# Performance work log

Measured on AMD Instinct MI355X. Metric: run time of the kernel, lower is better.

## Reference

```python
import jax, jax.numpy as jnp
import numpy as np

E, K, H, I = 64, 8, 2048, 768  # num_experts, top_k, hidden, moe_intermediate

def setup_inputs() -> dict:
    key = jax.random.key(0)
    k1, k2, k3, k4 = jax.random.split(key, 4)
    return {
        "hidden_states": jax.random.normal(k1, (1, 1024, H), dtype=jnp.float32),
        "w_gate": jax.random.normal(k2, (H, E), dtype=jnp.float32) * 0.02,
        "w13": jax.random.normal(k3, (E, H, 2 * I), dtype=jnp.float32) * 0.02,  # fused gate+up proj
        "w2": jax.random.normal(k4, (E, I, H), dtype=jnp.float32) * 0.02,
    }

def reference(hidden_states, w_gate, w13, w2):
    orig_shape = hidden_states.shape
    x = hidden_states.reshape(-1, orig_shape[-1])            # [T, H]
    T = x.shape[0]

    # Router: logits -> softmax -> top-k -> renormalize (norm_topk_prob=True)
    router_logits = x @ w_gate                               # [T, E]
    probs = jax.nn.softmax(router_logits, axis=-1)
    topk_w, topk_idx = jax.lax.top_k(probs, K)               # [T, K]
    topk_w = topk_w / jnp.sum(topk_w, axis=-1, keepdims=True)
    # Dense combine-weight matrix [T, E] (zero for non-routed experts)
    combine = jnp.zeros((T, E), dtype=x.dtype).at[
        jnp.arange(T)[:, None], topk_idx].add(topk_w)

    # Expert SwiGLU FFN, computed densely for all experts, masked by combine
    h = jnp.einsum('th,ehd->etd', x, w13)                    # [E, T, 2I]
    gate, up = h[..., :I], h[..., I:]
    act = jax.nn.silu(gate) * up                             # [E, T, I]
    y = jnp.einsum('eti,eih->eth', act, w2)                  # [E, T, H]
    out = jnp.einsum('eth,te->th', y, combine)               # [T, H]
    return out.reshape(orig_shape)
```

## Files before the change

### kernel.cpp

```cpp
#include <hip/hip_runtime.h>
#include <hip/hip_bf16.h>
#include <math.h>

#define NE 64
#define NK 8
#define NH 2048
#define NI 768
#define NT 1024
#define APITCH 40

typedef float f32x4 __attribute__((ext_vector_type(4)));
typedef __bf16 bf16x8 __attribute__((ext_vector_type(8)));
typedef __bf16 bf16x4 __attribute__((ext_vector_type(4)));

__global__ __launch_bounds__(256) void router_k(
    const float* __restrict__ x, const float* __restrict__ wg,
    __bf16* __restrict__ x_bf, int* __restrict__ topk_idx,
    float* __restrict__ topk_w)
{
    __shared__ float xs[4][NH];
    const int wave = threadIdx.x >> 6;
    const int lane = threadIdx.x & 63;
    const int t = blockIdx.x * 4 + wave;

    const float* xrow = x + (size_t)t * NH;
    __bf16* brow = x_bf + (size_t)t * NH;
    #pragma unroll
    for (int j = 0; j < 8; ++j) {
        int idx = j * 256 + lane * 4;
        f32x4 v = *reinterpret_cast<const f32x4*>(xrow + idx);
        *reinterpret_cast<f32x4*>(&xs[wave][idx]) = v;
        bf16x4 b;
        b[0] = (__bf16)v.x; b[1] = (__bf16)v.y; b[2] = (__bf16)v.z; b[3] = (__bf16)v.w;
        *reinterpret_cast<bf16x4*>(brow + idx) = b;
    }
    __syncthreads();

    float a0 = 0.f, a1 = 0.f, a2 = 0.f, a3 = 0.f;
    for (int h = 0; h < NH; h += 4) {
        a0 = fmaf(xs[wave][h + 0], wg[(h + 0) * NE + lane], a0);
        a1 = fmaf(xs[wave][h + 1], wg[(h + 1) * NE + lane], a1);
        a2 = fmaf(xs[wave][h + 2], wg[(h + 2) * NE + lane], a2);
        a3 = fmaf(xs[wave][h + 3], wg[(h + 3) * NE + lane], a3);
    }
    float acc = (a0 + a1) + (a2 + a3);

    float cur = acc;
    float sel_v[NK]; int sel_i[NK];
    #pragma unroll
    for (int k = 0; k < NK; ++k) {
        float bv = cur; int bi = lane;
        #pragma unroll
        for (int s = 32; s; s >>= 1) {
            float ov = __shfl_xor(bv, s, 64);
            int   oi = __shfl_xor(bi, s, 64);
            if (ov > bv || (ov == bv && oi < bi)) { bv = ov; bi = oi; }
        }
        sel_v[k] = bv; sel_i[k] = bi;
        if (lane == bi) cur = -3.4e38f;
    }
    float m = sel_v[0];
    float ssum = 0.f;
    #pragma unroll
    for (int k = 0; k < NK; ++k) ssum += expf(sel_v[k] - m);

    if (lane < NK) {
        float w = expf(sel_v[lane] - m) / ssum;
        topk_idx[t * NK + lane] = sel_i[lane];
        topk_w[t * NK + lane] = w;
    }
}

__global__ __launch_bounds__(256) void scanscatter_k(
    const int* __restrict__ topk_idx, const float* __restrict__ topk_w,
    int* __restrict__ counts, int* __restrict__ offs,
    int* __restrict__ slot_tok, float* __restrict__ slot_w,
    int* __restrict__ slot_of)
{
    __shared__ int hist[NE], base[NE], cur[NE];
    const int tid = threadIdx.x;
    if (tid < NE) hist[tid] = 0;
    __syncthreads();
    for (int i = tid; i < NT * NK; i += 256)
        atomicAdd(&hist[topk_idx[i]], 1);
    __syncthreads();
    if (tid == 0) {
        int r = 0;
        for (int e = 0; e < NE; ++e) { base[e] = r; r += hist[e]; }
    }
    __syncthreads();
    if (tid < NE) { counts[tid] = hist[tid]; offs[tid] = base[tid]; cur[tid] = 0; }
    __syncthreads();
    for (int i = tid; i < NT * NK; i += 256) {
        int e = topk_idx[i];
        int p = atomicAdd(&cur[e], 1);
        int g = base[e] + p;
        slot_tok[g] = i >> 3;
        slot_w[g] = topk_w[i];
        slot_of[i] = g;
    }
}

__global__ __launch_bounds__(256, 2) void e1_k(
    const __bf16* __restrict__ x_bf, const float* __restrict__ w13,
    const int* __restrict__ counts, const int* __restrict__ offs,
    const int* __restrict__ slot_tok, __bf16* __restrict__ act)
{
    const int e = blockIdx.x;
    const int cnt = counts[e];
    const int m0 = blockIdx.z * 256;
    if (m0 >= cnt) return;
    const int rows = min(256, cnt - m0);
    const int n0 = blockIdx.y * 64;
    const int goff = offs[e] + m0;

    __shared__ __bf16 A[2][256 * APITCH];
    __shared__ __bf16 B[2][128 * APITCH];
    __shared__ int tok[256];

    const int tid = threadIdx.x;
    tok[tid] = (tid < rows) ? slot_tok[goff + tid] : 0;
    __syncthreads();

    const int wave = tid >> 6, lane = tid & 63;
    f32x4 acc[4][8];
    #pragma unroll
    for (int i = 0; i < 4; ++i)
        #pragma unroll
        for (int j = 0; j < 8; ++j) acc[i][j] = (f32x4){0.f, 0.f, 0.f, 0.f};

    const float* w13e = w13 + (size_t)e * NH * (2 * NI);
    const int cc = tid & 31, kch = tid >> 5;
    const int bcol0 = cc * 4;
    const int gcol = (bcol0 < 64) ? (n0 + bcol0) : (NI + n0 + bcol0 - 64);
    const int rot = (cc >> 1) & 3;

    const __bf16* aptr[4];
    int aoff[4];
    bool aok[4];
    #pragma unroll
    for (int it = 0; it < 4; ++it) {
        int item = it * 256 + tid;
        int r = item >> 2, ch = item & 3;
        aptr[it] = x_bf + (size_t)tok[r] * NH + ch * 8;
        aoff[it] = r * APITCH + ch * 8;
        aok[it] = (r < rows);
    }
    const float* bptr = w13e + (size_t)(kch * 4) * (2 * NI) + gcol;
    int bcol[4], boff[4];
    #pragma unroll
    for (int jj = 0; jj < 4; ++jj) {
        int j = (jj + rot) & 3;
        bcol[jj] = j;
        boff[jj] = (bcol0 + j) * APITCH + kch * 4;
    }

    bf16x8 aReg[4];
    f32x4 bReg[4];

    auto loadT = [&](int kk) {
        #pragma unroll
        for (int it = 0; it < 4; ++it)
            if (aok[it]) aReg[it] = *reinterpret_cast<const bf16x8*>(aptr[it] + kk);
        #pragma unroll
        for (int ki = 0; ki < 4; ++ki)
            bReg[ki] = *reinterpret_cast<const f32x4*>(bptr + (size_t)(kk + ki) * (2 * NI));
    };
    auto writeT = [&](int buf) {
        #pragma unroll
        for (int it = 0; it < 4; ++it)
            if (aok[it]) *reinterpret_cast<bf16x8*>(&A[buf][aoff[it]]) = aReg[it];
        #pragma unroll
        for (int jj = 0; jj < 4; ++jj) {
            int j = bcol[jj];
            bf16x4 p;
            p[0] = (__bf16)bReg[0][j]; p[1] = (__bf16)bReg[1][j];
            p[2] = (__bf16)bReg[2][j]; p[3] = (__bf16)bReg[3][j];
            *reinterpret_cast<bf16x4*>(&B[buf][boff[jj]]) = p;
        }
    };
    auto compute = [&](int buf) {
        bf16x8 bfr[8];
        #pragma unroll
        for (int nf = 0; nf < 8; ++nf) {
            int col = nf * 16 + (lane & 15);
            bfr[nf] = *reinterpret_cast<const bf16x8*>(
                &B[buf][col * APITCH + (lane >> 4) * 8]);
        }
        #pragma unroll
        for (int mf = 0; mf < 4; ++mf) {
            int rf = mf * 64 + wave * 16;
            if (rf < rows) {
                int row = rf + (lane & 15);
                bf16x8 a = *reinterpret_cast<const bf16x8*>(
                    &A[buf][row * APITCH + (lane >> 4) * 8]);
                #pragma unroll
                for (int nf = 0; nf < 8; ++nf)
                    acc[mf][nf] = __builtin_amdgcn_mfma_f32_16x16x32_bf16(
                        a, bfr[nf], acc[mf][nf], 0, 0, 0);
            }
        }
    };

    loadT(0);
    writeT(0);
    __syncthreads();

    #pragma unroll 1
    for (int t = 0; t < 64; ++t) {
        if (t + 1 < 64) loadT((t + 1) * 32);
        compute(t & 1);
        if (t + 1 < 64) writeT((t + 1) & 1);
        __syncthreads();
    }

    #pragma unroll
    for (int mf = 0; mf < 4; ++mf) {
        int rf = mf * 64 + wave * 16;
        if (rf >= rows) continue;
        #pragma unroll
        for (int nf = 0; nf < 4; ++nf) {
            f32x4 g = acc[mf][nf];
            f32x4 u = acc[mf][nf + 4];
            int col = n0 + nf * 16 + (lane & 15);
            #pragma unroll
            for (int r = 0; r < 4; ++r) {
                int row = rf + ((lane >> 4) << 2) + r;
                if (row < rows) {
                    float gv = g[r];
                    float a = gv / (1.f + expf(-gv)) * u[r];
                    act[(size_t)(goff + row) * NI + col] = (__bf16)a;
                }
            }
        }
    }
}

__global__ __launch_bounds__(256, 2) void e2_k(
    const __bf16* __restrict__ act, const float* __restrict__ w2,
    const int* __restrict__ counts, const int* __restrict__ offs,
    const float* __restrict__ slot_w, __bf16* __restrict__ partial)
{
    const int e = blockIdx.x;
    const int cnt = counts[e];
    const int m0 = blockIdx.z * 256;
    if (m0 >= cnt) return;
    const int rows = min(256, cnt - m0);
    const int n0 = blockIdx.y * 128;
    const int goff = offs[e] + m0;

    __shared__ __bf16 A[2][256 * APITCH];
    __shared__ __bf16 B[2][128 * APITCH];

    const int tid = threadIdx.x, wave = tid >> 6, lane = tid & 63;
    f32x4 acc[4][8];
    #pragma unroll
    for (int i = 0; i < 4; ++i)
        #pragma unroll
        for (int j = 0; j < 8; ++j) acc[i][j] = (f32x4){0.f, 0.f, 0.f, 0.f};

    const float* w2e = w2 + (size_t)e * NI * NH;
    const int cc = tid & 31, kch = tid >> 5;
    const int bcol0 = cc * 4;
    const int rot = (cc >> 1) & 3;

    const __bf16* aptr[4];
    int aoff[4];
    bool aok[4];
    #pragma unroll
    for (int it = 0; it < 4; ++it) {
        int item = it * 256 + tid;
        int r = item >> 2, ch = item & 3;
        aptr[it] = act + (size_t)(goff + r) * NI + ch * 8;
        aoff[it] = r * APITCH + ch * 8;
        aok[it] = (r < rows);
    }
    const float* bptr = w2e + (size_t)(kch * 4) * NH + n0 + bcol0;
    int bcol[4], boff[4];
    #pragma unroll
    for (int jj = 0; jj < 4; ++jj) {
        int j = (jj + rot) & 3;
        bcol[jj] = j;
        boff[jj] = (bcol0 + j) * APITCH + kch * 4;
    }

    bf16x8 aReg[4];
    f32x4 bReg[4];

    auto loadT = [&](int kk) {
        #pragma unroll
        for (int it = 0; it < 4; ++it)
            if (aok[it]) aReg[it] = *reinterpret_cast<const bf16x8*>(aptr[it] + kk);
        #pragma unroll
        for (int ki = 0; ki < 4; ++ki)
            bReg[ki] = *reinterpret_cast<const f32x4*>(bptr + (size_t)(kk + ki) * NH);
    };
    auto writeT = [&](int buf) {
        #pragma unroll
        for (int it = 0; it < 4; ++it)
            if (aok[it]) *reinterpret_cast<bf16x8*>(&A[buf][aoff[it]]) = aReg[it];
        #pragma unroll
        for (int jj = 0; jj < 4; ++jj) {
            int j = bcol[jj];
            bf16x4 p;
            p[0] = (__bf16)bReg[0][j]; p[1] = (__bf16)bReg[1][j];
            p[2] = (__bf16)bReg[2][j]; p[3] = (__bf16)bReg[3][j];
            *reinterpret_cast<bf16x4*>(&B[buf][boff[jj]]) = p;
        }
    };
    auto compute = [&](int buf) {
        bf16x8 bfr[8];
        #pragma unroll
        for (int nf = 0; nf < 8; ++nf) {
            int col = nf * 16 + (lane & 15);
            bfr[nf] = *reinterpret_cast<const bf16x8*>(
                &B[buf][col * APITCH + (lane >> 4) * 8]);
        }
        #pragma unroll
        for (int mf = 0; mf < 4; ++mf) {
            int rf = mf * 64 + wave * 16;
            if (rf < rows) {
                int row = rf + (lane & 15);
                bf16x8 a = *reinterpret_cast<const bf16x8*>(
                    &A[buf][row * APITCH + (lane >> 4) * 8]);
                #pragma unroll
                for (int nf = 0; nf < 8; ++nf)
                    acc[mf][nf] = __builtin_amdgcn_mfma_f32_16x16x32_bf16(
                        a, bfr[nf], acc[mf][nf], 0, 0, 0);
            }
        }
    };

    loadT(0);
    writeT(0);
    __syncthreads();

    #pragma unroll 1
    for (int t = 0; t < 24; ++t) {
        if (t + 1 < 24) loadT((t + 1) * 32);
        compute(t & 1);
        if (t + 1 < 24) writeT((t + 1) & 1);
        __syncthreads();
    }

    #pragma unroll
    for (int mf = 0; mf < 4; ++mf) {
        int rf = mf * 64 + wave * 16;
        if (rf >= rows) continue;
        int rb = rf + ((lane >> 4) << 2);
        #pragma unroll
        for (int r = 0; r < 4; ++r) {
            int row = rb + r;
            if (row >= rows) continue;
            int gs = goff + row;
            float wv = slot_w[gs];
            #pragma unroll
            for (int nf = 0; nf < 8; ++nf) {
                int col = n0 + nf * 16 + (lane & 15);
                partial[(size_t)gs * NH + col] = (__bf16)(wv * acc[mf][nf][r]);
            }
        }
    }
}

__global__ __launch_bounds__(256) void combine_k(
    const __bf16* __restrict__ partial, const int* __restrict__ slot_of,
    float* __restrict__ out)
{
    const int t = blockIdx.x;
    const int c0 = threadIdx.x * 8;
    __shared__ int gs[NK];
    if (threadIdx.x < NK) gs[threadIdx.x] = slot_of[t * NK + threadIdx.x];
    __syncthreads();

    float s[8] = {0.f, 0.f, 0.f, 0.f, 0.f, 0.f, 0.f, 0.f};
    #pragma unroll
    for (int k = 0; k < NK; ++k) {
        bf16x8 v = *reinterpret_cast<const bf16x8*>(partial + (size_t)gs[k] * NH + c0);
        #pragma unroll
        for (int j = 0; j < 8; ++j) s[j] += (float)v[j];
    }
    f32x4 o0 = {s[0], s[1], s[2], s[3]};
    f32x4 o1 = {s[4], s[5], s[6], s[7]};
    *reinterpret_cast<f32x4*>(out + (size_t)t * NH + c0) = o0;
    *reinterpret_cast<f32x4*>(out + (size_t)t * NH + c0 + 4) = o1;
}

extern "C" void kernel_launch(void* const* d_in, const int* in_sizes, int n_in,
                              void* d_out, int out_size, void* d_ws, size_t ws_size,
                              hipStream_t stream)
{
    const float* x   = (const float*)d_in[0];
    const float* wg  = (const float*)d_in[1];
    const float* w13 = (const float*)d_in[2];
    const float* w2  = (const float*)d_in[3];
    float* out = (float*)d_out;
    char* ws = (char*)d_ws;

    __bf16* x_bf = (__bf16*)ws;
    size_t o = (size_t)4 * 1024 * 1024;
    __bf16* act = (__bf16*)(ws + o);      o += (size_t)8192 * NI * 2;
    __bf16* partial = (__bf16*)(ws + o);  o += (size_t)8192 * NH * 2;
    int*   topk_idx = (int*)(ws + o);     o += 8192 * 4;
    float* topk_w   = (float*)(ws + o);   o += 8192 * 4;
    int*   slot_tok = (int*)(ws + o);     o += 8192 * 4;
    float* slot_w   = (float*)(ws + o);   o += 8192 * 4;
    int*   slot_of  = (int*)(ws + o);     o += 8192 * 4;
    int*   counts   = (int*)(ws + o);     o += 256;
    int*   offs     = (int*)(ws + o);     o += 256;

    router_k    <<<NT / 4, 256, 0, stream>>>(x, wg, x_bf, topk_idx, topk_w);
    scanscatter_k<<<1, 256, 0, stream>>>(topk_idx, topk_w, counts, offs,
                                         slot_tok, slot_w, slot_of);
    e1_k<<<dim3(NE, NI / 64, 2), 256, 0, stream>>>(x_bf, w13, counts, offs, slot_tok, act);
    e2_k<<<dim3(NE, NH / 128, 2), 256, 0, stream>>>(act, w2, counts, offs, slot_w, partial);
    combine_k<<<NT, 256, 0, stream>>>(partial, slot_of, out);
}
```

Before: 438.4 us.

## Load A fragments directly from global and double K-step per LDS stage

```diff
diff --git a/kernel.cpp b/kernel.cpp
--- a/kernel.cpp
+++ b/kernel.cpp
@@ -7,7 +7,8 @@
 #define NH 2048
 #define NI 768
 #define NT 1024
-#define APITCH 40
+#define BP 40
+#define BSUB (128 * BP)
 
 typedef float f32x4 __attribute__((ext_vector_type(4)));
 typedef __bf16 bf16x8 __attribute__((ext_vector_type(8)));
@@ -114,12 +115,11 @@
     const int n0 = blockIdx.y * 64;
     const int goff = offs[e] + m0;
 
-    __shared__ __bf16 A[2][256 * APITCH];
-    __shared__ __bf16 B[2][128 * APITCH];
+    __shared__ __bf16 B[2][2 * BSUB];
     __shared__ int tok[256];
 
     const int tid = threadIdx.x;
-    tok[tid] = (tid < rows) ? slot_tok[goff + tid] : 0;
+    tok[tid] = (tid < rows) ? slot_tok[goff + tid] : slot_tok[goff];
     __syncthreads();
 
     const int wave = tid >> 6, lane = tid & 63;
@@ -128,78 +128,76 @@
     for (int i = 0; i < 4; ++i)
         #pragma unroll
         for (int j = 0; j < 8; ++j) acc[i][j] = (f32x4){0.f, 0.f, 0.f, 0.f};
+
+    const __bf16* ap[4];
+    bool mok[4];
+    #pragma unroll
+    for (int mf = 0; mf < 4; ++mf) {
+        int rf = mf * 64 + wave * 16;
+        mok[mf] = (rf < rows);
+        int arow = rf + (lane & 15);
+        ap[mf] = x_bf + (size_t)tok[arow] * NH + ((lane >> 4) << 3);
+    }
 
     const float* w13e = w13 + (size_t)e * NH * (2 * NI);
     const int cc = tid & 31, kch = tid >> 5;
     const int bcol0 = cc * 4;
     const int gcol = (bcol0 < 64) ? (n0 + bcol0) : (NI + n0 + bcol0 - 64);
     const int rot = (cc >> 1) & 3;
-
-    const __bf16* aptr[4];
-    int aoff[4];
-    bool aok[4];
-    #pragma unroll
-    for (int it = 0; it < 4; ++it) {
-        int item = it * 256 + tid;
-        int r = item >> 2, ch = item & 3;
-        aptr[it] = x_bf + (size_t)tok[r] * NH + ch * 8;
-        aoff[it] = r * APITCH + ch * 8;
-        aok[it] = (r < rows);
-    }
     const float* bptr = w13e + (size_t)(kch * 4) * (2 * NI) + gcol;
-    int bcol[4], boff[4];
+    int bj[4], boff[4];
     #pragma unroll
     for (int jj = 0; jj < 4; ++jj) {
         int j = (jj + rot) & 3;
-        bcol[jj] = j;
-        boff[jj] = (bcol0 + j) * APITCH + kch * 4;
-    }
-
-    bf16x8 aReg[4];
-    f32x4 bReg[4];
-
+        bj[jj] = j;
+        boff[jj] = (bcol0 + j) * BP + kch * 4;
+    }
+
+    f32x4 bReg[2][4];
     auto loadT = [&](int kk) {
         #pragma unroll
-        for (int it = 0; it < 4; ++it)
-            if (aok[it]) aReg[it] = *reinterpret_cast<const bf16x8*>(aptr[it] + kk);
-        #pragma unroll
-        for (int ki = 0; ki < 4; ++ki)
-            bReg[ki] = *reinterpret_cast<const f32x4*>(bptr + (size_t)(kk + ki) * (2 * NI));
+        for (int s = 0; s < 2; ++s)
+            #pragma unroll
+            for (int ki = 0; ki < 4; ++ki)
+                bReg[s][ki] = *reinterpret_cast<const f32x4*>(
+                    bptr + (size_t)(kk + s * 32 + ki) * (2 * NI));
     };
     auto writeT = [&](int buf) {
         #pragma unroll
-        for (int it = 0; it < 4; ++it)
-            if (aok[it]) *reinterpret_cast<bf16x8*>(&A[buf][aoff[it]]) = aReg[it];
-        #pragma unroll
-        for (int jj = 0; jj < 4; ++jj) {
-            int j = bcol[jj];
-            bf16x4 p;
-            p[0] = (__bf16)bReg[0][j]; p[1] = (__bf16)bReg[1][j];
-            p[2] = (__bf16)bReg[2][j]; p[3] = (__bf16)bReg[3][j];
-            *reinterpret_cast<bf16x4*>(&B[buf][boff[jj]]) = p;
+        for (int s = 0; s < 2; ++s)
+            #pragma unroll
+            for (int jj = 0; jj < 4; ++jj) {
+                int j = bj[jj];
+                bf16x4 p;
+                p[0] = (__bf16)bReg[s][0][j]; p[1] = (__bf16)bReg[s][1][j];
+                p[2] = (__bf16)bReg[s][2][j]; p[3] = (__bf16)bReg[s][3][j];
+                *reinterpret_cast<bf16x4*>(&B[buf][s * BSUB + boff[jj]]) = p;
+            }
+    };
+    auto compute = [&](int buf) {
+        #pragma unroll
+        for (int kk = 0; kk < 2; ++kk) {
+            bf16x8 av[4];
+            #pragma unroll
+            for (int mf = 0; mf < 4; ++mf)
+                if (mok[mf]) av[mf] = *reinterpret_cast<const bf16x8*>(ap[mf] + kk * 32);
+            bf16x8 bfr[8];
+            #pragma unroll
+            for (int nf = 0; nf < 8; ++nf) {
+                int col = nf * 16 + (lane & 15);
+                bfr[nf] = *reinterpret_cast<const bf16x8*>(
+                    &B[buf][kk * BSUB + col * BP + ((lane >> 4) << 3)]);
+            }
+            #pragma unroll
+            for (int mf = 0; mf < 4; ++mf)
+                if (mok[mf])
+                    #pragma unroll
+                    for (int nf = 0; nf < 8; ++nf)
+                        acc[mf][nf] = __builtin_amdgcn_mfma_f32_16x16x32_bf16(
+                            av[mf], bfr[nf], acc[mf][nf], 0, 0, 0);
         }
-    };
-    auto compute = [&](int buf) {
-        bf16x8 bfr[8];
-        #pragma unroll
-        for (int nf = 0; nf < 8; ++nf) {
-            int col = nf * 16 + (lane & 15);
-            bfr[nf] = *reinterpret_cast<const bf16x8*>(
-                &B[buf][col * APITCH + (lane >> 4) * 8]);
-        }
-        #pragma unroll
-        for (int mf = 0; mf < 4; ++mf) {
-            int rf = mf * 64 + wave * 16;
-            if (rf < rows) {
-                int row = rf + (lane & 15);
-                bf16x8 a = *reinterpret_cast<const bf16x8*>(
-                    &A[buf][row * APITCH + (lane >> 4) * 8]);
-                #pragma unroll
-                for (int nf = 0; nf < 8; ++nf)
-                    acc[mf][nf] = __builtin_amdgcn_mfma_f32_16x16x32_bf16(
-                        a, bfr[nf], acc[mf][nf], 0, 0, 0);
-            }
-        }
+        #pragma unroll
+        for (int mf = 0; mf < 4; ++mf) ap[mf] += 64;
     };
 
     loadT(0);
@@ -207,10 +205,10 @@
     __syncthreads();
 
     #pragma unroll 1
-    for (int t = 0; t < 64; ++t) {
-        if (t + 1 < 64) loadT((t + 1) * 32);
+    for (int t = 0; t < 32; ++t) {
+        if (t + 1 < 32) loadT((t + 1) * 64);
         compute(t & 1);
-        if (t + 1 < 64) writeT((t + 1) & 1);
+        if (t + 1 < 32) writeT((t + 1) & 1);
         __syncthreads();
     }
 
@@ -249,8 +247,7 @@
     const int n0 = blockIdx.y * 128;
     const int goff = offs[e] + m0;
 
-    __shared__ __bf16 A[2][256 * APITCH];
-    __shared__ __bf16 B[2][128 * APITCH];
+    __shared__ __bf16 B[2][2 * BSUB];
 
     const int tid = threadIdx.x, wave = tid >> 6, lane = tid & 63;
     f32x4 acc[4][8];
@@ -258,77 +255,75 @@
     for (int i = 0; i < 4; ++i)
         #pragma unroll
         for (int j = 0; j < 8; ++j) acc[i][j] = (f32x4){0.f, 0.f, 0.f, 0.f};
+
+    const __bf16* ap[4];
+    bool mok[4];
+    #pragma unroll
+    for (int mf = 0; mf < 4; ++mf) {
+        int rf = mf * 64 + wave * 16;
+        mok[mf] = (rf < rows);
+        int arow = goff + rf + (lane & 15);
+        ap[mf] = act + (size_t)arow * NI + ((lane >> 4) << 3);
+    }
 
     const float* w2e = w2 + (size_t)e * NI * NH;
     const int cc = tid & 31, kch = tid >> 5;
     const int bcol0 = cc * 4;
     const int rot = (cc >> 1) & 3;
-
-    const __bf16* aptr[4];
-    int aoff[4];
-    bool aok[4];
-    #pragma unroll
-    for (int it = 0; it < 4; ++it) {
-        int item = it * 256 + tid;
-        int r = item >> 2, ch = item & 3;
-        aptr[it] = act + (size_t)(goff + r) * NI + ch * 8;
-        aoff[it] = r * APITCH + ch * 8;
-        aok[it] = (r < rows);
-    }
     const float* bptr = w2e + (size_t)(kch * 4) * NH + n0 + bcol0;
-    int bcol[4], boff[4];
+    int bj[4], boff[4];
     #pragma unroll
     for (int jj = 0; jj < 4; ++jj) {
         int j = (jj + rot) & 3;
-        bcol[jj] = j;
-        boff[jj] = (bcol0 + j) * APITCH + kch * 4;
-    }
-
-    bf16x8 aReg[4];
-    f32x4 bReg[4];
-
+        bj[jj] = j;
+        boff[jj] = (bcol0 + j) * BP + kch * 4;
+    }
+
+    f32x4 bReg[2][4];
     auto loadT = [&](int kk) {
         #pragma unroll
-        for (int it = 0; it < 4; ++it)
-            if (aok[it]) aReg[it] = *reinterpret_cast<const bf16x8*>(aptr[it] + kk);
-        #pragma unroll
-        for (int ki = 0; ki < 4; ++ki)
-            bReg[ki] = *reinterpret_cast<const f32x4*>(bptr + (size_t)(kk + ki) * NH);
+        for (int s = 0; s < 2; ++s)
+            #pragma unroll
+            for (int ki = 0; ki < 4; ++ki)
+                bReg[s][ki] = *reinterpret_cast<const f32x4*>(
+                    bptr + (size_t)(kk + s * 32 + ki) * NH);
     };
     auto writeT = [&](int buf) {
         #pragma unroll
-        for (int it = 0; it < 4; ++it)
-            if (aok[it]) *reinterpret_cast<bf16x8*>(&A[buf][aoff[it]]) = aReg[it];
-        #pragma unroll
-        for (int jj = 0; jj < 4; ++jj) {
-            int j = bcol[jj];
-            bf16x4 p;
-            p[0] = (__bf16)bReg[0][j]; p[1] = (__bf16)bReg[1][j];
-            p[2] = (__bf16)bReg[2][j]; p[3] = (__bf16)bReg[3][j];
-            *reinterpret_cast<bf16x4*>(&B[buf][boff[jj]]) = p;
+        for (int s = 0; s < 2; ++s)
+            #pragma unroll
+            for (int jj = 0; jj < 4; ++jj) {
+                int j = bj[jj];
+                bf16x4 p;
+                p[0] = (__bf16)bReg[s][0][j]; p[1] = (__bf16)bReg[s][1][j];
+                p[2] = (__bf16)bReg[s][2][j]; p[3] = (__bf16)bReg[s][3][j];
+                *reinterpret_cast<bf16x4*>(&B[buf][s * BSUB + boff[jj]]) = p;
+            }
+    };
+    auto compute = [&](int buf) {
+        #pragma unroll
+        for (int kk = 0; kk < 2; ++kk) {
+            bf16x8 av[4];
+            #pragma unroll
+            for (int mf = 0; mf < 4; ++mf)
+                if (mok[mf]) av[mf] = *reinterpret_cast<const bf16x8*>(ap[mf] + kk * 32);
+            bf16x8 bfr[8];
+            #pragma unroll
+            for (int nf = 0; nf < 8; ++nf) {
+                int col = nf * 16 + (lane & 15);
+                bfr[nf] = *reinterpret_cast<const bf16x8*>(
+                    &B[buf][kk * BSUB + col * BP + ((lane >> 4) << 3)]);
+            }
+            #pragma unroll
+            for (int mf = 0; mf < 4; ++mf)
+                if (mok[mf])
+                    #pragma unroll
+                    for (int nf = 0; nf < 8; ++nf)
+                        acc[mf][nf] = __builtin_amdgcn_mfma_f32_16x16x32_bf16(
+                            av[mf], bfr[nf], acc[mf][nf], 0, 0, 0);
         }
-    };
-    auto compute = [&](int buf) {
-        bf16x8 bfr[8];
-        #pragma unroll
-        for (int nf = 0; nf < 8; ++nf) {
-            int col = nf * 16 + (lane & 15);
-            bfr[nf] = *reinterpret_cast<const bf16x8*>(
-                &B[buf][col * APITCH + (lane >> 4) * 8]);
-        }
-        #pragma unroll
-        for (int mf = 0; mf < 4; ++mf) {
-            int rf = mf * 64 + wave * 16;
-            if (rf < rows) {
-                int row = rf + (lane & 15);
-                bf16x8 a = *reinterpret_cast<const bf16x8*>(
-                    &A[buf][row * APITCH + (lane >> 4) * 8]);
-                #pragma unroll
-                for (int nf = 0; nf < 8; ++nf)
-                    acc[mf][nf] = __builtin_amdgcn_mfma_f32_16x16x32_bf16(
-                        a, bfr[nf], acc[mf][nf], 0, 0, 0);
-            }
-        }
+        #pragma unroll
+        for (int mf = 0; mf < 4; ++mf) ap[mf] += 64;
     };
 
     loadT(0);
@@ -336,10 +331,10 @@
     __syncthreads();
 
     #pragma unroll 1
-    for (int t = 0; t < 24; ++t) {
-        if (t + 1 < 24) loadT((t + 1) * 32);
+    for (int t = 0; t < 12; ++t) {
+        if (t + 1 < 12) loadT((t + 1) * 64);
         compute(t & 1);
-        if (t + 1 < 24) writeT((t + 1) & 1);
+        if (t + 1 < 12) writeT((t + 1) & 1);
         __syncthreads();
     }
 
```

Measured after the change: 441.7 us. About the same (+0.7%).
